# Kernel optimization log

Hardware: AMD Instinct MI355X
Metric: run time of the kernel (lower is better)

Reference implementation:

```python
import jax, jax.numpy as jnp
import numpy as np
from jax import lax

B, H, W_IN, C = 32, 32, 32, 128   # NHWC input
KH, KW = 3, 3                     # kernel size (padding 'same', stride 1)
F = 512                           # filters


def setup_inputs() -> dict:
    key = jax.random.key(0)
    ks = jax.random.split(key, 10)
    # sparse factor shapes: (KH*KW*C, 1152), (1152, F), (F, F)
    d0, d1, d2, d3 = KH * KW * C, 1152, F, F
    x = jax.random.normal(ks[0], (B, H, W_IN, C), dtype=jnp.float32)
    k0 = jax.random.normal(ks[1], (d0, d1), dtype=jnp.float32) * (1.0 / np.sqrt(d0))
    k1 = jax.random.normal(ks[2], (d1, d2), dtype=jnp.float32) * (1.0 / np.sqrt(d1))
    k2 = jax.random.normal(ks[3], (d2, d3), dtype=jnp.float32) * (1.0 / np.sqrt(d2))
    # fixed binary sparsity masks (K.constant in the original build)
    m0 = jax.random.bernoulli(ks[4], 0.1, (d0, d1)).astype(jnp.float32)
    m1 = jax.random.bernoulli(ks[5], 0.1, (d1, d2)).astype(jnp.float32)
    m2 = jax.random.bernoulli(ks[6], 0.1, (d2, d3)).astype(jnp.float32)
    scale = jax.random.normal(ks[7], (1,), dtype=jnp.float32)
    bias = jax.random.normal(ks[8], (F,), dtype=jnp.float32) * 0.01
    return {"x": x, "k0": k0, "k1": k1, "k2": k2,
            "m0": m0, "m1": m1, "m2": m2, "scale": scale, "bias": bias}


def reference(x, k0, k1, k2, m0, m1, m2, scale, bias):
    # Chained masked sparse factors collapse (associativity) to one effective
    # filter matrix of shape (KH*KW*C, F); the im2col row flatten order in the
    # original is (h, w, c), which matches an HWIO reshape exactly.
    w_eff = (k0 * m0) @ (k1 * m1) @ (k2 * m2)          # (KH*KW*C, F)
    w = (w_eff * scale[0]).reshape(KH, KW, C, F)        # fold scalar scale into kernel
    out = lax.conv_general_dilated(
        x, w, window_strides=(1, 1), padding='SAME',
        dimension_numbers=('NHWC', 'HWIO', 'NHWC'))     # (B, H, W, F)
    return out + bias
```

## Files before the change

### kernel.cpp

```cpp
#include <hip/hip_runtime.h>

typedef __attribute__((ext_vector_type(8))) short short8;
typedef __attribute__((ext_vector_type(4))) float f32x4;

typedef __attribute__((address_space(1))) const unsigned gas_u32;
typedef __attribute__((address_space(3))) unsigned las_u32;

static __device__ __forceinline__ void g2l16(const void* g, void* l) {
  __builtin_amdgcn_global_load_lds((gas_u32*)g, (las_u32*)l, 16, 0, 0);
}

static __device__ __forceinline__ short f2bf(float f) {
  union { float f; unsigned u; } v; v.f = f;
  unsigned r = (v.u + 0x7FFFu + ((v.u >> 16) & 1u)) >> 16;
  return (short)r;
}

__global__ __launch_bounds__(256) void k_prep(const float* __restrict__ x,
                                              const float* __restrict__ k0f,
                                              const float* __restrict__ m0f,
                                              const float* __restrict__ scf,
                                              const float* __restrict__ k1f,
                                              const float* __restrict__ m1f,
                                              const float* __restrict__ k2f,
                                              const float* __restrict__ m2f,
                                              short* __restrict__ xbp,
                                              short* __restrict__ w1b,
                                              short* __restrict__ w2T,
                                              short* __restrict__ w3T) {
  __shared__ float tile[32][33];
  const int bb = blockIdx.x, tid = threadIdx.x;
  if (bb < 648) {
    int i = bb * 256 + tid;
    float s = scf[0];
    const f32x4* kk = (const f32x4*)k0f + (size_t)i * 2;
    const f32x4* mm = (const f32x4*)m0f + (size_t)i * 2;
    f32x4 a0 = kk[0], a1 = kk[1], b0 = mm[0], b1 = mm[1];
    short8 o;
    o[0] = f2bf(a0[0] * b0[0] * s); o[1] = f2bf(a0[1] * b0[1] * s);
    o[2] = f2bf(a0[2] * b0[2] * s); o[3] = f2bf(a0[3] * b0[3] * s);
    o[4] = f2bf(a1[0] * b1[0] * s); o[5] = f2bf(a1[1] * b1[1] * s);
    o[6] = f2bf(a1[2] * b1[2] * s); o[7] = f2bf(a1[3] * b1[3] * s);
    ((short8*)w1b)[i] = o;
  } else if (bb < 1480) {
    const float *kf, *mf; short* outp; int D, F, idx;
    if (bb < 1224) { kf = k1f; mf = m1f; outp = w2T; D = 1152; F = 512; idx = bb - 648; }
    else           { kf = k2f; mf = m2f; outp = w3T; D = 512;  F = 512; idx = bb - 1224; }
    int f0 = (idx & 15) * 32, d0 = (idx >> 4) * 32;
    int tx = tid & 31, ty = tid >> 5;
#pragma unroll
    for (int i = 0; i < 4; ++i) {
      int d = d0 + ty + i * 8;
      size_t ix = (size_t)d * F + f0 + tx;
      tile[ty + i * 8][tx] = kf[ix] * mf[ix];
    }
    __syncthreads();
#pragma unroll
    for (int i = 0; i < 4; ++i) {
      int f = f0 + ty + i * 8;
      outp[(size_t)f * D + d0 + tx] = f2bf(tile[tx][ty + i * 8]);
    }
  } else {
    int i = (bb - 1480) * 256 + tid;
    int c8 = i & 15;
    int t = i >> 4;
    int wp = t % 34, t2 = t / 34;
    int hp = t2 % 34, b = t2 / 34;
    short8 o = {};
    if (hp >= 1 && hp <= 32 && wp >= 1 && wp <= 32) {
      const f32x4* s = (const f32x4*)(x + (((size_t)((b << 5) + hp - 1) << 5) + (wp - 1)) * 128 + c8 * 8);
      f32x4 a = s[0], bb2 = s[1];
      o[0] = f2bf(a[0]); o[1] = f2bf(a[1]); o[2] = f2bf(a[2]); o[3] = f2bf(a[3]);
      o[4] = f2bf(bb2[0]); o[5] = f2bf(bb2[1]); o[6] = f2bf(bb2[2]); o[7] = f2bf(bb2[3]);
    }
    ((short8*)xbp)[i] = o;
  }
}

__global__ __launch_bounds__(256) void k_gemm64(const short* __restrict__ A,
                                                const short* __restrict__ BT,
                                                short* __restrict__ C, int M, int N, int K) {
  __shared__ __align__(16) short As[64][64];
  __shared__ __align__(16) short Bs[64][64];
  const int ntiles = N >> 6;
  const int m0 = (blockIdx.x / ntiles) << 6, n0 = (blockIdx.x % ntiles) << 6;
  const int tid = threadIdx.x;
  const int lane = tid & 63, wv = tid >> 6;
  const int wr = (wv >> 1) * 32, wc = (wv & 1) * 32;
  const int lr = lane & 15, lk = (lane >> 4) * 8;

  f32x4 acc[2][2] = {};

  const int rr = tid >> 3, c8 = (tid & 7) * 8;
  unsigned abase[2], bbase[2];
#pragma unroll
  for (int j = 0; j < 2; ++j) {
    abase[j] = (unsigned)(m0 + j * 32 + rr) * K + c8;
    bbase[j] = (unsigned)(n0 + j * 32 + rr) * K + c8;
  }
  short* AsL = &As[0][0];
  short* BsL = &Bs[0][0];
  const int lo = wv * 512;

  for (int kt = 0; kt < K; kt += 64) {
#pragma unroll
    for (int j = 0; j < 2; ++j) g2l16(A + abase[j] + kt, AsL + j * 2048 + lo);
#pragma unroll
    for (int j = 0; j < 2; ++j) g2l16(BT + bbase[j] + kt, BsL + j * 2048 + lo);
    __syncthreads();
#pragma unroll
    for (int ks = 0; ks < 2; ++ks) {
      const int ko = ks * 32 + lk;
      short8 af[2], bf[2];
#pragma unroll
      for (int i = 0; i < 2; ++i) af[i] = *(const short8*)&As[wr + i * 16 + lr][ko];
#pragma unroll
      for (int i = 0; i < 2; ++i) bf[i] = *(const short8*)&Bs[wc + i * 16 + lr][ko];
#pragma unroll
      for (int mi = 0; mi < 2; ++mi)
#pragma unroll
        for (int ni = 0; ni < 2; ++ni)
          acc[mi][ni] = __builtin_amdgcn_mfma_f32_16x16x32_bf16(af[mi], bf[ni], acc[mi][ni], 0, 0, 0);
    }
    __syncthreads();
  }
#pragma unroll
  for (int mi = 0; mi < 2; ++mi) {
    const int row = m0 + wr + mi * 16 + (lane >> 4) * 4;
#pragma unroll
    for (int ni = 0; ni < 2; ++ni) {
      const int col = n0 + wc + ni * 16 + lr;
#pragma unroll
      for (int q = 0; q < 4; ++q)
        C[(size_t)(row + q) * N + col] = f2bf(acc[mi][ni][q]);
    }
  }
}

#define MF(a_, b_, c_) __builtin_amdgcn_mfma_f32_16x16x32_bf16(a_, b_, c_, 0, 0, 0)

#define RD_A(bu_, mf_, ks_) \
  (*(const short8*)&As[bu_][wr * 128 + (mf_) * 16 + lr][(((ks_) * 4 + lh) ^ (lr & 7)) * 8])
#define RD_B(bu_, nf_, ks_) \
  (*(const short8*)&Bs[bu_][wc * 64 + (nf_) * 16 + lr][(((ks_) * 4 + lh) ^ (lr & 7)) * 8])

#define LOADB4(bu_) do { \
  bfr[0][0] = RD_B(bu_, 0, 0); bfr[0][1] = RD_B(bu_, 0, 1); \
  bfr[1][0] = RD_B(bu_, 1, 0); bfr[1][1] = RD_B(bu_, 1, 1); \
  bfr[2][0] = RD_B(bu_, 2, 0); bfr[2][1] = RD_B(bu_, 2, 1); \
  bfr[3][0] = RD_B(bu_, 3, 0); bfr[3][1] = RD_B(bu_, 3, 1); } while (0)

#define STAGE_AQ(q_, tt_) do { \
  const int tc_ = (tt_) > 17 ? 17 : (tt_); \
  const int khw_ = tc_ >> 1; const int kh_ = (khw_ * 11) >> 5; const int kw_ = khw_ - kh_ * 3; \
  const int ao_ = (kh_ * 34 + kw_) * 128 + ((tc_ & 1) << 6) + (q_) * 4352; \
  g2l16(xbp + aBase + ao_, &As[tc_ & 1][aRow + (q_) * 32][0]); } while (0)

#define STAGE_BQ(q_, tt_) do { \
  const int tc_ = (tt_) > 17 ? 17 : (tt_); \
  g2l16(wT + bBase + (q_) * 73728 + tc_ * 64, &Bs[tc_ & 1][bRow + (q_) * 64][0]); } while (0)

#define MFMA16(p_) \
  acc[2*(p_)  ][0] = MF(a0k0, bfr[0][0], acc[2*(p_)  ][0]); \
  acc[2*(p_)  ][1] = MF(a0k0, bfr[1][0], acc[2*(p_)  ][1]); \
  acc[2*(p_)  ][2] = MF(a0k0, bfr[2][0], acc[2*(p_)  ][2]); \
  acc[2*(p_)  ][3] = MF(a0k0, bfr[3][0], acc[2*(p_)  ][3]); \
  acc[2*(p_)+1][0] = MF(a1k0, bfr[0][0], acc[2*(p_)+1][0]); \
  acc[2*(p_)+1][1] = MF(a1k0, bfr[1][0], acc[2*(p_)+1][1]); \
  acc[2*(p_)+1][2] = MF(a1k0, bfr[2][0], acc[2*(p_)+1][2]); \
  acc[2*(p_)+1][3] = MF(a1k0, bfr[3][0], acc[2*(p_)+1][3]); \
  acc[2*(p_)  ][0] = MF(a0k1, bfr[0][1], acc[2*(p_)  ][0]); \
  acc[2*(p_)  ][1] = MF(a0k1, bfr[1][1], acc[2*(p_)  ][1]); \
  acc[2*(p_)  ][2] = MF(a0k1, bfr[2][1], acc[2*(p_)  ][2]); \
  acc[2*(p_)  ][3] = MF(a0k1, bfr[3][1], acc[2*(p_)  ][3]); \
  acc[2*(p_)+1][0] = MF(a1k1, bfr[0][1], acc[2*(p_)+1][0]); \
  acc[2*(p_)+1][1] = MF(a1k1, bfr[1][1], acc[2*(p_)+1][1]); \
  acc[2*(p_)+1][2] = MF(a1k1, bfr[2][1], acc[2*(p_)+1][2]); \
  acc[2*(p_)+1][3] = MF(a1k1, bfr[3][1], acc[2*(p_)+1][3]);

#define PHASE(bu_, p_, PRE, TT_, WAITV) do { \
  PRE; \
  short8 a0k0 = RD_A(bu_, 2*(p_), 0),   a0k1 = RD_A(bu_, 2*(p_), 1); \
  short8 a1k0 = RD_A(bu_, 2*(p_)+1, 0), a1k1 = RD_A(bu_, 2*(p_)+1, 1); \
  __builtin_amdgcn_s_barrier(); \
  asm volatile("s_waitcnt lgkmcnt(0)" ::: "memory"); \
  __builtin_amdgcn_sched_barrier(0); \
  STAGE_AQ(p_, TT_); \
  STAGE_BQ(p_, TT_); \
  __builtin_amdgcn_s_setprio(1); \
  MFMA16(p_) \
  __builtin_amdgcn_s_setprio(0); \
  WAITV; \
  __builtin_amdgcn_s_barrier(); \
} while (0)

#define VM8 asm volatile("s_waitcnt vmcnt(8)" ::: "memory")

__global__ __launch_bounds__(512, 2) void k_conv(const short* __restrict__ xbp,
                                                 const short* __restrict__ wT,
                                                 const float* __restrict__ bias,
                                                 float* __restrict__ out) {
  __shared__ __align__(16) short As[2][256][64];
  __shared__ __align__(16) short Bs[2][256][64];
  int bid = blockIdx.x;
  bid = (bid & 7) * 32 + (bid >> 3);
  const int mt = bid >> 1, nt = bid & 1;
  const int m0 = mt << 8, n0 = nt << 8;
  const int tid = threadIdx.x;
  const int lane = tid & 63, wid = tid >> 6;
  const int wr = wid >> 2, wc = wid & 3;
  const int lr = lane & 15, lh = lane >> 4;

  f32x4 acc[8][4] = {};
  short8 bfr[4][2];

  const int wrB = (wid >> 2) * 128;
  const int rsub = (wid & 3) * 8 + (lane >> 3);
  const int sw = (lane & 7) ^ (lane >> 3);
  const int aRow = wrB + (wid & 3) * 8;
  const int bRow = wid * 8;

  const int Mb = m0 + wrB + rsub;
  const int b = Mb >> 10, h0 = (Mb >> 5) & 31, w = Mb & 31;
  const unsigned aBase = (unsigned)((b * 34 + h0) * 34 + w) * 128 + sw * 8;
  const unsigned bBase = (unsigned)(n0 + wid * 8 + (lane >> 3)) * 1152 + sw * 8;

  STAGE_AQ(0, 0); STAGE_BQ(0, 0); STAGE_AQ(1, 0); STAGE_BQ(1, 0);
  STAGE_AQ(2, 0); STAGE_BQ(2, 0); STAGE_AQ(3, 0); STAGE_BQ(3, 0);
  STAGE_AQ(0, 1); STAGE_BQ(0, 1); STAGE_AQ(1, 1); STAGE_BQ(1, 1);
  STAGE_AQ(2, 1); STAGE_BQ(2, 1); STAGE_AQ(3, 1); STAGE_BQ(3, 1);
  VM8;
  __builtin_amdgcn_s_barrier();

  for (int it = 0; it < 9; ++it) {
    const int ta = 2 * it;
    PHASE(0, 0, LOADB4(0), ta + 2, );
    PHASE(0, 1, ,          ta + 2, );
    PHASE(0, 2, ,          ta + 2, );
    PHASE(0, 3, ,          ta + 2, VM8);
    PHASE(1, 0, LOADB4(1), ta + 3, );
    PHASE(1, 1, ,          ta + 3, );
    PHASE(1, 2, ,          ta + 3, );
    PHASE(1, 3, ,          ta + 3, VM8);
  }
  asm volatile("s_waitcnt vmcnt(0)" ::: "memory");

  const int orow = m0 + wr * 128, ocol = n0 + wc * 64;
#pragma unroll
  for (int mf = 0; mf < 8; ++mf) {
    const int row = orow + mf * 16 + lh * 4;
#pragma unroll
    for (int nf = 0; nf < 4; ++nf) {
      const int col = ocol + nf * 16 + lr;
      const float bv = bias[col];
#pragma unroll
      for (int q = 0; q < 4; ++q)
        out[(size_t)(row + q) * 512 + col] = acc[mf][nf][q] + bv;
    }
  }
}

extern "C" void kernel_launch(void* const* d_in, const int* in_sizes, int n_in,
                              void* d_out, int out_size, void* d_ws, size_t ws_size,
                              hipStream_t stream) {
  (void)in_sizes; (void)n_in; (void)out_size; (void)ws_size;
  const float* x    = (const float*)d_in[0];
  const float* k0   = (const float*)d_in[1];
  const float* k1   = (const float*)d_in[2];
  const float* k2   = (const float*)d_in[3];
  const float* m0   = (const float*)d_in[4];
  const float* m1   = (const float*)d_in[5];
  const float* m2   = (const float*)d_in[6];
  const float* sc   = (const float*)d_in[7];
  const float* bias = (const float*)d_in[8];
  float* out = (float*)d_out;
  char* ws = (char*)d_ws;

  short* xbp = (short*)(ws);
  short* w1b = (short*)(ws + 9469952);
  short* w2T = (short*)(ws + 12124160);
  short* w3T = (short*)(ws + 13303808);
  short* A1b = (short*)(ws + 13828096);
  short* wET = (short*)(ws + 15007744);

  k_prep<<<3792, 256, 0, stream>>>(x, k0, m0, sc, k1, m1, k2, m2, xbp, w1b, w2T, w3T);
  k_gemm64<<<144, 256, 0, stream>>>(w1b, w2T, A1b, 1152, 512, 1152);
  k_gemm64<<<144, 256, 0, stream>>>(w3T, A1b, wET, 512, 1152, 512);
  k_conv<<<256, 512, 0, stream>>>(xbp, wET, bias, out);
}
```

Measured before the change: 79.41 us.

## Shrink conv tile to 256x128 with single-buffered LDS and more resident blocks

The implicit-GEMM conv kernel now uses a 256x128 output tile instead of 256x256 and launches 512 blocks instead of 256. LDS drops from double-buffered A and B to a single A buffer plus a half-size B buffer. Each phase reads its A rows into registers and then refills the same rows with the next k-step in place, and launch bounds now allow four blocks per CU. The aim is to put more blocks on each CU and cut per-block register and LDS use so memory latency is better hidden. In exchange, each A tile is loaded twice as often and each MFMA phase does half as much work between barriers.

Measured after the change: 76.17 us. 4.1% less time.

```diff
diff --git a/kernel.cpp b/kernel.cpp
--- a/kernel.cpp
+++ b/kernel.cpp
@@ -139,80 +139,70 @@
 
 #define MF(a_, b_, c_) __builtin_amdgcn_mfma_f32_16x16x32_bf16(a_, b_, c_, 0, 0, 0)
 
-#define RD_A(bu_, mf_, ks_) \
-  (*(const short8*)&As[bu_][wr * 128 + (mf_) * 16 + lr][(((ks_) * 4 + lh) ^ (lr & 7)) * 8])
-#define RD_B(bu_, nf_, ks_) \
-  (*(const short8*)&Bs[bu_][wc * 64 + (nf_) * 16 + lr][(((ks_) * 4 + lh) ^ (lr & 7)) * 8])
-
-#define LOADB4(bu_) do { \
-  bfr[0][0] = RD_B(bu_, 0, 0); bfr[0][1] = RD_B(bu_, 0, 1); \
-  bfr[1][0] = RD_B(bu_, 1, 0); bfr[1][1] = RD_B(bu_, 1, 1); \
-  bfr[2][0] = RD_B(bu_, 2, 0); bfr[2][1] = RD_B(bu_, 2, 1); \
-  bfr[3][0] = RD_B(bu_, 3, 0); bfr[3][1] = RD_B(bu_, 3, 1); } while (0)
+#define RD_A(mf_, ks_) \
+  (*(const short8*)&As[wr * 128 + (mf_) * 16 + lr][(((ks_) * 4 + lh) ^ (lr & 7)) * 8])
+#define RD_B(nf_, ks_) \
+  (*(const short8*)&Bs[wc * 32 + (nf_) * 16 + lr][(((ks_) * 4 + lh) ^ (lr & 7)) * 8])
+
+#define LOADB do { \
+  bfr[0][0] = RD_B(0, 0); bfr[0][1] = RD_B(0, 1); \
+  bfr[1][0] = RD_B(1, 0); bfr[1][1] = RD_B(1, 1); } while (0)
 
 #define STAGE_AQ(q_, tt_) do { \
   const int tc_ = (tt_) > 17 ? 17 : (tt_); \
   const int khw_ = tc_ >> 1; const int kh_ = (khw_ * 11) >> 5; const int kw_ = khw_ - kh_ * 3; \
   const int ao_ = (kh_ * 34 + kw_) * 128 + ((tc_ & 1) << 6) + (q_) * 4352; \
-  g2l16(xbp + aBase + ao_, &As[tc_ & 1][aRow + (q_) * 32][0]); } while (0)
-
-#define STAGE_BQ(q_, tt_) do { \
+  g2l16(xbp + aBase + ao_, &As[aRow + (q_) * 32][0]); } while (0)
+
+#define STAGE_BH(j_, tt_) do { \
   const int tc_ = (tt_) > 17 ? 17 : (tt_); \
-  g2l16(wT + bBase + (q_) * 73728 + tc_ * 64, &Bs[tc_ & 1][bRow + (q_) * 64][0]); } while (0)
-
-#define MFMA16(p_) \
+  g2l16(wT + bBase + (j_) * 73728 + tc_ * 64, &Bs[(j_) * 64 + bRow][0]); } while (0)
+
+#define MFMA8(p_) \
   acc[2*(p_)  ][0] = MF(a0k0, bfr[0][0], acc[2*(p_)  ][0]); \
   acc[2*(p_)  ][1] = MF(a0k0, bfr[1][0], acc[2*(p_)  ][1]); \
-  acc[2*(p_)  ][2] = MF(a0k0, bfr[2][0], acc[2*(p_)  ][2]); \
-  acc[2*(p_)  ][3] = MF(a0k0, bfr[3][0], acc[2*(p_)  ][3]); \
   acc[2*(p_)+1][0] = MF(a1k0, bfr[0][0], acc[2*(p_)+1][0]); \
   acc[2*(p_)+1][1] = MF(a1k0, bfr[1][0], acc[2*(p_)+1][1]); \
-  acc[2*(p_)+1][2] = MF(a1k0, bfr[2][0], acc[2*(p_)+1][2]); \
-  acc[2*(p_)+1][3] = MF(a1k0, bfr[3][0], acc[2*(p_)+1][3]); \
   acc[2*(p_)  ][0] = MF(a0k1, bfr[0][1], acc[2*(p_)  ][0]); \
   acc[2*(p_)  ][1] = MF(a0k1, bfr[1][1], acc[2*(p_)  ][1]); \
-  acc[2*(p_)  ][2] = MF(a0k1, bfr[2][1], acc[2*(p_)  ][2]); \
-  acc[2*(p_)  ][3] = MF(a0k1, bfr[3][1], acc[2*(p_)  ][3]); \
   acc[2*(p_)+1][0] = MF(a1k1, bfr[0][1], acc[2*(p_)+1][0]); \
-  acc[2*(p_)+1][1] = MF(a1k1, bfr[1][1], acc[2*(p_)+1][1]); \
-  acc[2*(p_)+1][2] = MF(a1k1, bfr[2][1], acc[2*(p_)+1][2]); \
-  acc[2*(p_)+1][3] = MF(a1k1, bfr[3][1], acc[2*(p_)+1][3]);
-
-#define PHASE(bu_, p_, PRE, TT_, WAITV) do { \
+  acc[2*(p_)+1][1] = MF(a1k1, bfr[1][1], acc[2*(p_)+1][1]);
+
+#define PHASE(p_, PRE, WAITV, ...) do { \
   PRE; \
-  short8 a0k0 = RD_A(bu_, 2*(p_), 0),   a0k1 = RD_A(bu_, 2*(p_), 1); \
-  short8 a1k0 = RD_A(bu_, 2*(p_)+1, 0), a1k1 = RD_A(bu_, 2*(p_)+1, 1); \
+  short8 a0k0 = RD_A(2*(p_), 0),   a0k1 = RD_A(2*(p_), 1); \
+  short8 a1k0 = RD_A(2*(p_)+1, 0), a1k1 = RD_A(2*(p_)+1, 1); \
   __builtin_amdgcn_s_barrier(); \
   asm volatile("s_waitcnt lgkmcnt(0)" ::: "memory"); \
   __builtin_amdgcn_sched_barrier(0); \
-  STAGE_AQ(p_, TT_); \
-  STAGE_BQ(p_, TT_); \
+  __VA_ARGS__ \
   __builtin_amdgcn_s_setprio(1); \
-  MFMA16(p_) \
+  MFMA8(p_) \
   __builtin_amdgcn_s_setprio(0); \
   WAITV; \
   __builtin_amdgcn_s_barrier(); \
 } while (0)
 
-#define VM8 asm volatile("s_waitcnt vmcnt(8)" ::: "memory")
-
-__global__ __launch_bounds__(512, 2) void k_conv(const short* __restrict__ xbp,
+#define VM5 asm volatile("s_waitcnt vmcnt(5)" ::: "memory")
+#define VM3 asm volatile("s_waitcnt vmcnt(3)" ::: "memory")
+
+__global__ __launch_bounds__(512, 4) void k_conv(const short* __restrict__ xbp,
                                                  const short* __restrict__ wT,
                                                  const float* __restrict__ bias,
                                                  float* __restrict__ out) {
-  __shared__ __align__(16) short As[2][256][64];
-  __shared__ __align__(16) short Bs[2][256][64];
+  __shared__ __align__(16) short As[256][64];
+  __shared__ __align__(16) short Bs[128][64];
   int bid = blockIdx.x;
-  bid = (bid & 7) * 32 + (bid >> 3);
-  const int mt = bid >> 1, nt = bid & 1;
-  const int m0 = mt << 8, n0 = nt << 8;
+  bid = (bid & 7) * 64 + (bid >> 3);
+  const int mt = bid >> 2, nt = bid & 3;
+  const int m0 = mt << 8, n0 = nt << 7;
   const int tid = threadIdx.x;
   const int lane = tid & 63, wid = tid >> 6;
   const int wr = wid >> 2, wc = wid & 3;
   const int lr = lane & 15, lh = lane >> 4;
 
-  f32x4 acc[8][4] = {};
-  short8 bfr[4][2];
+  f32x4 acc[8][2] = {};
+  short8 bfr[2][2];
 
   const int wrB = (wid >> 2) * 128;
   const int rsub = (wid & 3) * 8 + (lane >> 3);
@@ -225,32 +215,26 @@
   const unsigned aBase = (unsigned)((b * 34 + h0) * 34 + w) * 128 + sw * 8;
   const unsigned bBase = (unsigned)(n0 + wid * 8 + (lane >> 3)) * 1152 + sw * 8;
 
-  STAGE_AQ(0, 0); STAGE_BQ(0, 0); STAGE_AQ(1, 0); STAGE_BQ(1, 0);
-  STAGE_AQ(2, 0); STAGE_BQ(2, 0); STAGE_AQ(3, 0); STAGE_BQ(3, 0);
-  STAGE_AQ(0, 1); STAGE_BQ(0, 1); STAGE_AQ(1, 1); STAGE_BQ(1, 1);
-  STAGE_AQ(2, 1); STAGE_BQ(2, 1); STAGE_AQ(3, 1); STAGE_BQ(3, 1);
-  VM8;
+  STAGE_BH(0, 0); STAGE_BH(1, 0);
+  STAGE_AQ(0, 0); STAGE_AQ(1, 0); STAGE_AQ(2, 0); STAGE_AQ(3, 0);
+  asm volatile("s_waitcnt vmcnt(0)" ::: "memory");
   __builtin_amdgcn_s_barrier();
 
-  for (int it = 0; it < 9; ++it) {
-    const int ta = 2 * it;
-    PHASE(0, 0, LOADB4(0), ta + 2, );
-    PHASE(0, 1, ,          ta + 2, );
-    PHASE(0, 2, ,          ta + 2, );
-    PHASE(0, 3, ,          ta + 2, VM8);
-    PHASE(1, 0, LOADB4(1), ta + 3, );
-    PHASE(1, 1, ,          ta + 3, );
-    PHASE(1, 2, ,          ta + 3, );
-    PHASE(1, 3, ,          ta + 3, VM8);
+  for (int t = 0; t < 18; ++t) {
+    const int tn = t + 1;
+    PHASE(0, LOADB, VM5, STAGE_BH(0, tn); STAGE_BH(1, tn); STAGE_AQ(0, tn););
+    PHASE(1, ,      VM5, STAGE_AQ(1, tn););
+    PHASE(2, ,      VM5, STAGE_AQ(2, tn););
+    PHASE(3, ,      VM3, STAGE_AQ(3, tn););
   }
   asm volatile("s_waitcnt vmcnt(0)" ::: "memory");
 
-  const int orow = m0 + wr * 128, ocol = n0 + wc * 64;
+  const int orow = m0 + wr * 128, ocol = n0 + wc * 32;
 #pragma unroll
   for (int mf = 0; mf < 8; ++mf) {
     const int row = orow + mf * 16 + lh * 4;
 #pragma unroll
-    for (int nf = 0; nf < 4; ++nf) {
+    for (int nf = 0; nf < 2; ++nf) {
       const int col = ocol + nf * 16 + lr;
       const float bv = bias[col];
 #pragma unroll
@@ -286,5 +270,5 @@
   k_prep<<<3792, 256, 0, stream>>>(x, k0, m0, sc, k1, m1, k2, m2, xbp, w1b, w2T, w3T);
   k_gemm64<<<144, 256, 0, stream>>>(w1b, w2T, A1b, 1152, 512, 1152);
   k_gemm64<<<144, 256, 0, stream>>>(w3T, A1b, wET, 512, 1152, 512);
-  k_conv<<<256, 512, 0, stream>>>(xbp, wET, bias, out);
-}
+  k_conv<<<512, 512, 0, stream>>>(xbp, wET, bias, out);
+}
```
